# Kernel tuning notes

Measured on AMD Instinct MI355X. Metric: run time of the kernel, lower is better.

## Reference

```python
import jax, jax.numpy as jnp
import numpy as np
import math

B, N, D = 8, 4096, 256
Q = 0.5
K = 8  # max_order
EPS = 1e-5


def scale_norm(x, g):
    n = jnp.linalg.norm(x, axis=-1, keepdims=True)
    return g * x / jnp.maximum(n, EPS)


def siren(x, w1, b1, g, w2, b2):
    # nn.Linear uses y = x @ W.T + b with W [out, in]
    h = jnp.sin(jnp.einsum('bnd,ed->bne', x, w1) + b1)
    h = scale_norm(h, g)
    return jnp.sin(jnp.einsum('bnd,ed->bne', h, w2) + b2)


def adaptive_avg_pool6(x):
    # AdaptiveAvgPool1d(6) over last dim (torch semantics: bin j = mean(x[floor(jL/6):ceil((j+1)L/6)]))
    L = x.shape[-1]
    cols = []
    for j in range(6):
        s = (j * L) // 6
        e = -((-(j + 1) * L) // 6)
        cols.append(jnp.mean(x[..., s:e], axis=-1))
    return jnp.stack(cols, axis=-1)


def jackson_damp(k_max):
    c = math.pi / (k_max + 2)
    k = np.arange(k_max + 1)
    d = ((k_max + 2 - k) * math.sin(c) * np.cos(k * c) + math.cos(c) * np.sin(k * c)) / ((k_max + 2) * math.sin(c))
    d[0] = 1.0
    return jnp.asarray(d, dtype=jnp.float32)


def cheb_gibbs(seq, coef, damp):
    # seq [B,N], coef [B,K+1], damp [K+1] (rows of module buffer are identical)
    out = coef[:, 0:1] + seq * coef[:, 1:2] * damp[1]
    tx0, tx1 = jnp.ones_like(seq), seq
    for k in range(2, K + 1):
        tx2 = 2.0 * seq * tx1 - tx0
        out = out + tx2 * coef[:, k:k + 1] * damp[k]
        tx0, tx1 = tx1, tx2
    return out


def givens(alpha, beta, gamma):
    ra = (alpha + beta) * (math.pi / 2.0)
    rs = (alpha - beta) * (math.pi / 2.0)
    gm = gamma * (math.pi / 2.0)
    cg, sg = jnp.cos(gm), jnp.sin(gm)
    g_ii = jnp.exp(-1j * ra) * cg
    g_ij = jnp.exp(-1j * rs) * sg
    g_ji = -jnp.exp(1j * rs) * sg
    g_jj = jnp.exp(1j * ra) * cg
    return g_ii, g_ij, g_ji, g_jj


def dhhp(x, li, lij, lji, ljj, ui, uij, uji, ujj, diag_pre=None, diag_post=None):
    # x [B,N,D] complex; Givens factors [B,N-1]. Banded Hessenberg transform Z = G_l (G_u x).
    if diag_pre is not None:
        x = diag_pre[:, :, None] * x
    y0 = ui[:, 0:1, None] * x[:, 0:1] + uij[:, 0:1, None] * x[:, 1:2]
    ym = (uji[:, :-1, None] * x[:, :-2]
          + (ujj[:, :-1] * ui[:, 1:])[:, :, None] * x[:, 1:-1]
          + (ujj[:, :-1] * uij[:, 1:])[:, :, None] * x[:, 2:])
    yl = uji[:, -1:, None] * x[:, -2:-1] + ujj[:, -1:, None] * x[:, -1:]
    Y = jnp.concatenate([y0, ym, yl], axis=1)
    z0 = li[:, 0:1, None] * Y[:, 0:1] + lij[:, 0:1, None] * Y[:, 1:2]
    zm = ((li[:, 1:] * lji[:, :-1])[:, :, None] * Y[:, :-2]
          + (li[:, 1:] * ljj[:, :-1])[:, :, None] * Y[:, 1:-1]
          + lij[:, 1:, None] * Y[:, 2:])
    zl = lji[:, -1:, None] * Y[:, -2:-1] + ljj[:, -1:, None] * Y[:, -1:]
    Z = jnp.concatenate([z0, zm, zl], axis=1)
    if diag_post is not None:
        Z = diag_post[:, :, None] * Z
    return Z


def chsyconv(x, ev_w1, ev_b1, ev_g, ev_w2, ev_b2, hp_w1, hp_b1, hp_g, hp_w2, hp_b2, cheb_coef):
    # eigenvalue hypernetwork: mean over feat dim (pool_dim=2) -> [B,N]
    eig = jnp.mean(siren(x, ev_w1, ev_b1, ev_g, ev_w2, ev_b2), axis=2)
    filt = cheb_gibbs(eig, cheb_coef, jackson_damp(K))  # KPM-filtered eigenvalues
    diag = filt.astype(jnp.complex64) * jnp.exp(2j * math.pi * Q * eig)  # magnetic complex diagonal
    # eigenvector hyperparameters: pool feat->6, view [B,6N], chunk into 6 along dim 1
    pooled = adaptive_avg_pool6(siren(x, hp_w1, hp_b1, hp_g, hp_w2, hp_b2)).reshape(B, 6 * N)
    a_l, b_l, g_l, a_u, b_u, g_u = jnp.split(pooled, 6, axis=1)
    l_ii, l_ij, l_ji, l_jj = givens(a_l[:, 1:], b_l[:, 1:], g_l[:, 1:])
    u_ii, u_ij, u_ji, u_jj = givens(a_u[:, :-1], b_u[:, :-1], g_u[:, :-1])
    xc = x.astype(jnp.complex64)
    # DHHP transform (transform=True): diagonal filter applied after the banded transform
    Z = dhhp(xc, l_ii, l_ij, l_ji, l_jj, u_ii, u_ij, u_ji, u_jj, diag_post=diag)
    # inverse DHHP: conjugate-transpose Givens factors (ii<->jj, ij->-ij, ji->-ji), no diagonal
    out = dhhp(Z, l_jj, -l_ij, -l_ji, l_ii, u_jj, -u_ij, -u_ji, u_ii)
    return out  # complex64 [B,N,D] (value dropout is identity in eval)


def setup_inputs():
    key = jax.random.key(0)
    ks = jax.random.split(key, 5)
    bound = math.sqrt(6.0 / D)
    x = jax.random.normal(ks[0], (B, N, D), dtype=jnp.float32)
    ev_w1 = jax.random.uniform(ks[1], (D, D), jnp.float32, -bound, bound)
    ev_w2 = jax.random.uniform(ks[2], (D, D), jnp.float32, -bound, bound)
    hp_w1 = jax.random.uniform(ks[3], (D, D), jnp.float32, -bound, bound)
    hp_w2 = jax.random.uniform(ks[4], (D, D), jnp.float32, -bound, bound)
    zb = jnp.zeros((D,), jnp.float32)
    g = jnp.asarray(math.sqrt(D), jnp.float32)  # ScaleNorm scale init
    cheb_coef = jnp.full((B, K + 1), 2.0 / (K + 1), jnp.float32).at[:, 0].set(1.0 / (K + 1))
    return {"x": x, "ev_w1": ev_w1, "ev_b1": zb, "ev_g": g, "ev_w2": ev_w2, "ev_b2": zb,
            "hp_w1": hp_w1, "hp_b1": zb, "hp_g": g, "hp_w2": hp_w2, "hp_b2": zb,
            "cheb_coef": cheb_coef}


def reference(x, ev_w1, ev_b1, ev_g, ev_w2, ev_b2, hp_w1, hp_b1, hp_g, hp_w2, hp_b2, cheb_coef):
    return chsyconv(x, ev_w1, ev_b1, ev_g, ev_w2, ev_b2, hp_w1, hp_b1, hp_g, hp_w2, hp_b2, cheb_coef)
```

## Files before the change

### kernel.cpp

```cpp
#include <hip/hip_runtime.h>
#include <math.h>

typedef __attribute__((ext_vector_type(8))) _Float16 f16x8;
typedef __attribute__((ext_vector_type(4))) float    f32x4;

static constexpr int cB  = 8;
static constexpr int cN  = 4096;
static constexpr int cD  = 256;
static constexpr int cBN = cB * cN;
#define PI_F 3.14159265358979323846f

__device__ __forceinline__ float2 cmul(float2 a, float2 b) {
    return make_float2(a.x*b.x - a.y*b.y, a.x*b.y + a.y*b.x);
}
__device__ __forceinline__ float2 cfma2(float2 a, float2 b, float2 acc) {
    acc.x += a.x*b.x - a.y*b.y;
    acc.y += a.x*b.y + a.y*b.x;
    return acc;
}
__device__ __forceinline__ float2 cneg(float2 a) { return make_float2(-a.x, -a.y); }

struct G4 { float2 ii, ij, ji, jj; };

__device__ __forceinline__ G4 givens_f(float al, float be, float ga) {
    float ra = (al + be) * (PI_F * 0.5f);
    float rs = (al - be) * (PI_F * 0.5f);
    float gm = ga * (PI_F * 0.5f);
    float sg, cg, sra, cra, srs, crs;
    sincosf(gm, &sg, &cg);
    sincosf(ra, &sra, &cra);
    sincosf(rs, &srs, &crs);
    G4 g;
    g.ii = make_float2( cra*cg, -sra*cg);
    g.ij = make_float2( crs*sg, -srs*sg);
    g.ji = make_float2(-crs*sg, -srs*sg);
    g.jj = make_float2( cra*cg,  sra*cg);
    return g;
}

__global__ void sentinel_kernel(float* out, int n, float v) {
    if (n > 0) out[0] = v;
    if (n > 1) out[1] = v;
}

__global__ __launch_bounds__(256) void wcvt_kernel(
    const float* __restrict__ w0, const float* __restrict__ w1,
    const float* __restrict__ w2, const float* __restrict__ w3,
    _Float16* __restrict__ W16)
{
    int i = blockIdx.x * 256 + threadIdx.x;
    const float* src[4] = {w0, w1, w2, w3};
    #pragma unroll
    for (int m = 0; m < 4; ++m)
        W16[(size_t)m*65536 + i] = (_Float16)src[m][i];
}

__device__ __forceinline__ void stage_x16(const float* __restrict__ xrow0,
                                          _Float16* buf, int tid)
{
    const int row = tid >> 3;
    const int c0  = (tid & 7) * 32;
    const float4* src = (const float4*)(xrow0 + row*256 + c0);
    const int swz = (row & 7) << 4;
    #pragma unroll
    for (int j = 0; j < 4; ++j) {
        float4 p = src[2*j], q = src[2*j+1];
        f16x8 h;
        h[0]=(_Float16)p.x; h[1]=(_Float16)p.y; h[2]=(_Float16)p.z; h[3]=(_Float16)p.w;
        h[4]=(_Float16)q.x; h[5]=(_Float16)q.y; h[6]=(_Float16)q.z; h[7]=(_Float16)q.w;
        int off = (((c0 + j*8) * 2) ^ swz);
        *(f16x8*)((char*)buf + row*512 + off) = h;
    }
}

__device__ __forceinline__ void ld_a1(const _Float16* src, int k0, int lr, int kq,
                                      f16x8 ah[4])
{
    #pragma unroll
    for (int mt = 0; mt < 4; ++mt) {
        int row = mt*16 + lr;
        int off = ((k0*2 + kq*16) ^ ((row & 7) << 4));
        ah[mt] = *(const f16x8*)((const char*)src + row*512 + off);
    }
}

__device__ __forceinline__ void ld_w1(const _Float16* __restrict__ wP,
                                      int k0, int w, int lr, int kq, f16x8 bh[2])
{
    #pragma unroll
    for (int nt = 0; nt < 2; ++nt) {
        int col = w*32 + nt*16 + lr;
        bh[nt] = *(const f16x8*)(wP + col*256 + k0 + kq*8);
    }
}

__device__ __forceinline__ void do_mfma8(const f16x8 ah[4], const f16x8 bh[2],
                                         f32x4 acc[4][2])
{
    #pragma unroll
    for (int mt = 0; mt < 4; ++mt)
        #pragma unroll
        for (int nt = 0; nt < 2; ++nt)
            acc[mt][nt] = __builtin_amdgcn_mfma_f32_16x16x32_f16(ah[mt], bh[nt], acc[mt][nt], 0, 0, 0);
}

__device__ __forceinline__ void gemm32(const _Float16* aSrc,
                                       const _Float16* __restrict__ wP,
                                       int w, int lr, int kq, f32x4 acc[4][2])
{
    f16x8 ah[4];
    f16x8 b0[2], b1[2];
    ld_w1(wP, 0, w, lr, kq, b0);
    #pragma unroll
    for (int kk = 0; kk < 8; ++kk) {
        ld_a1(aSrc, kk*32, lr, kq, ah);
        if ((kk & 1) == 0) {
            if (kk < 7) ld_w1(wP, (kk+1)*32, w, lr, kq, b1);
            do_mfma8(ah, b0, acc);
        } else {
            if (kk < 7) ld_w1(wP, (kk+1)*32, w, lr, kq, b0);
            do_mfma8(ah, b1, acc);
        }
    }
}

__global__ __launch_bounds__(512, 2) void siren_mfma(
    const float* __restrict__ x, const _Float16* __restrict__ W16,
    const float* __restrict__ ev_b1, const float* __restrict__ ev_g,
    const float* __restrict__ ev_b2,
    const float* __restrict__ hp_b1, const float* __restrict__ hp_g,
    const float* __restrict__ hp_b2,
    const float* __restrict__ cheb,
    float* __restrict__ Pout, float2* __restrict__ DIAG)
{
    __shared__ _Float16 buf[64*256];
    __shared__ float red[8][64];

    const int tid  = threadIdx.x;
    const int w    = tid >> 6;
    const int lane = tid & 63;
    const int lr   = lane & 15;
    const int kq   = lane >> 4;
    const size_t r0 = (size_t)blockIdx.x * 64;
    const int b   = (int)(r0 >> 12);
    const int net = blockIdx.y;

    const _Float16* w1P = W16 + (size_t)(net*2 + 0)*65536;
    const _Float16* w2P = W16 + (size_t)(net*2 + 1)*65536;
    const float* b1 = net ? hp_b1 : ev_b1;
    const float* b2 = net ? hp_b2 : ev_b2;
    const float  g  = net ? hp_g[0] : ev_g[0];

    stage_x16(x + r0*256, buf, tid);
    __syncthreads();

    f32x4 acc[4][2];
    #pragma unroll
    for (int mt = 0; mt < 4; ++mt)
        #pragma unroll
        for (int nt = 0; nt < 2; ++nt) acc[mt][nt] = (f32x4)(0.f);
    gemm32(buf, w1P, w, lr, kq, acc);

    {
        float bv[2] = { b1[w*32 + lr], b1[w*32 + 16 + lr] };
        float sv[4][2][4], rn[4][4];
        #pragma unroll
        for (int mt = 0; mt < 4; ++mt)
            #pragma unroll
            for (int r = 0; r < 4; ++r) {
                float s = 0.f;
                #pragma unroll
                for (int nt = 0; nt < 2; ++nt) {
                    float v = __sinf(acc[mt][nt][r] + bv[nt]);
                    sv[mt][nt][r] = v;
                    s += v*v;
                }
                rn[mt][r] = s;
            }
        #pragma unroll
        for (int mk = 1; mk < 16; mk <<= 1)
            #pragma unroll
            for (int mt = 0; mt < 4; ++mt)
                #pragma unroll
                for (int r = 0; r < 4; ++r) rn[mt][r] += __shfl_xor(rn[mt][r], mk);
        if (lr == 0)
            #pragma unroll
            for (int mt = 0; mt < 4; ++mt)
                #pragma unroll
                for (int r = 0; r < 4; ++r) red[w][mt*16 + kq*4 + r] = rn[mt][r];
        __syncthreads();
        #pragma unroll
        for (int mt = 0; mt < 4; ++mt)
            #pragma unroll
            for (int r = 0; r < 4; ++r) {
                int row = mt*16 + kq*4 + r;
                float tot = 0.f;
                #pragma unroll
                for (int ww = 0; ww < 8; ++ww) tot += red[ww][row];
                float sc = g / fmaxf(sqrtf(tot), 1e-5f);
                int swz = (row & 7) << 4;
                #pragma unroll
                for (int nt = 0; nt < 2; ++nt) {
                    float v = sv[mt][nt][r] * sc;
                    int col = w*32 + nt*16 + lr;
                    *(_Float16*)((char*)buf + row*512 + ((col*2) ^ swz)) = (_Float16)v;
                }
            }
    }
    __syncthreads();

    #pragma unroll
    for (int mt = 0; mt < 4; ++mt)
        #pragma unroll
        for (int nt = 0; nt < 2; ++nt) acc[mt][nt] = (f32x4)(0.f);
    gemm32(buf, w2P, w, lr, kq, acc);

    if (net == 0) {
        float bv[2] = { b2[w*32 + lr], b2[w*32 + 16 + lr] };
        float es[4][4];
        #pragma unroll
        for (int mt = 0; mt < 4; ++mt)
            #pragma unroll
            for (int r = 0; r < 4; ++r) {
                float s = 0.f;
                #pragma unroll
                for (int nt = 0; nt < 2; ++nt) s += __sinf(acc[mt][nt][r] + bv[nt]);
                es[mt][r] = s;
            }
        #pragma unroll
        for (int mk = 1; mk < 16; mk <<= 1)
            #pragma unroll
            for (int mt = 0; mt < 4; ++mt)
                #pragma unroll
                for (int r = 0; r < 4; ++r) es[mt][r] += __shfl_xor(es[mt][r], mk);
        if (lr == 0)
            #pragma unroll
            for (int mt = 0; mt < 4; ++mt)
                #pragma unroll
                for (int r = 0; r < 4; ++r) red[w][mt*16 + kq*4 + r] = es[mt][r];
        __syncthreads();
        if (tid < 64) {
            int row = tid;
            float tot = 0.f;
            #pragma unroll
            for (int ww = 0; ww < 8; ++ww) tot += red[ww][row];
            float ev = tot * (1.f/256.f);
            float dmp[9];
            {
                const double c = 3.14159265358979323846 / 10.0;
                double sc = sin(c), cc = cos(c);
                dmp[0] = 1.f;
                for (int k = 1; k < 9; ++k)
                    dmp[k] = (float)(((10.0 - k) * sc * cos(k*c) + cc * sin(k*c)) / (10.0 * sc));
            }
            const float* cf = cheb + b*9;
            float t0 = 1.f, t1 = ev;
            float filt = cf[0] + ev * cf[1] * dmp[1];
            #pragma unroll
            for (int k = 2; k < 9; ++k) {
                float t2 = 2.f*ev*t1 - t0;
                filt += t2 * cf[k] * dmp[k];
                t0 = t1; t1 = t2;
            }
            float sp, cp;
            sincosf(PI_F * ev, &sp, &cp);
            DIAG[r0 + row] = make_float2(filt*cp, filt*sp);
        }
    } else {
        __syncthreads();
        float bv[2] = { b2[w*32 + lr], b2[w*32 + 16 + lr] };
        #pragma unroll
        for (int mt = 0; mt < 4; ++mt)
            #pragma unroll
            for (int r = 0; r < 4; ++r) {
                int row = mt*16 + kq*4 + r;
                int swz = (row & 7) << 4;
                #pragma unroll
                for (int nt = 0; nt < 2; ++nt) {
                    float v = __sinf(acc[mt][nt][r] + bv[nt]);
                    int col = w*32 + nt*16 + lr;
                    *(_Float16*)((char*)buf + row*512 + ((col*2) ^ swz)) = (_Float16)v;
                }
            }
        __syncthreads();
        if (tid < 384) {
            const int sb[6] = {0, 42, 85, 128, 170, 213};
            const int eb[6] = {43, 86, 128, 171, 214, 256};
            const float inv[6] = {1.f/43.f, 1.f/44.f, 1.f/43.f, 1.f/43.f, 1.f/44.f, 1.f/43.f};
            int row = tid / 6, q = tid - row*6;
            int swz = (row & 7) << 4;
            float s = 0.f;
            for (int c = sb[q]; c < eb[q]; ++c)
                s += (float)(*(const _Float16*)((const char*)buf + row*512 + ((c*2) ^ swz)));
            int nn = (int)(r0 & 4095) + row;
            Pout[(size_t)b*6*cN + nn*6 + q] = s * inv[q];
        }
    }
}

__global__ __launch_bounds__(256) void prep_T(
    const float* __restrict__ P, const float2* __restrict__ DIAG,
    float2* __restrict__ T)
{
    __shared__ G4 uL[266], lL[266];
    __shared__ float2 dgL[262];

    const int tid = threadIdx.x;
    const int m0 = (blockIdx.x & 15) * 256;
    const int b  = blockIdx.x >> 4;
    const size_t bbase = (size_t)b * cN;
    const int b6 = b * 6 * cN;
    const float2 z2 = make_float2(0.f, 0.f);
    const int jb = m0 - 5;

    for (int t = tid; t < 265; t += 256) {
        int j = jb + t;
        G4 gu, gl;
        gu.ii = gu.ij = gu.ji = gu.jj = z2; gl = gu;
        if (j >= 0 && j <= cN-2) {
            gu = givens_f(P[b6+3*cN+j], P[b6+4*cN+j], P[b6+5*cN+j]);
            gl = givens_f(P[b6+j+1],    P[b6+cN+j+1], P[b6+2*cN+j+1]);
        }
        uL[t] = gu; lL[t] = gl;
    }
    for (int t = tid; t < 261; t += 256) {
        int m = m0 - 2 + t;
        dgL[t] = (m >= 0 && m < cN) ? DIAG[bbase + m] : z2;
    }
    __syncthreads();

    const int m = m0 + tid;
    auto scoef = [&](int s, int rr, float2& A, float2& B, float2& C) {
        A = z2; B = z2; C = z2;
        if (rr < 0 || rr >= cN) return;
        if (s == 1) {
            if (rr == 0)         { G4 u0 = uL[0-jb]; B = u0.ii; C = u0.ij; }
            else if (rr == cN-1) { G4 up = uL[rr-1-jb]; A = up.ji; B = up.jj; }
            else { G4 up = uL[rr-1-jb], uc = uL[rr-jb];
                   A = up.ji; B = cmul(up.jj, uc.ii); C = cmul(up.jj, uc.ij); }
        } else if (s == 2) {
            if (rr == 0)         { G4 l0 = lL[0-jb]; B = l0.ii; C = l0.ij; }
            else if (rr == cN-1) { G4 lp = lL[rr-1-jb]; A = lp.ji; B = lp.jj; }
            else { G4 lp = lL[rr-1-jb], lc = lL[rr-jb];
                   A = cmul(lc.ii, lp.ji); B = cmul(lc.ii, lp.jj); C = lc.ij; }
        } else if (s == 3) {
            if (rr == 0)         { G4 u0 = uL[0-jb]; B = u0.jj; C = cneg(u0.ij); }
            else if (rr == cN-1) { G4 up = uL[rr-1-jb]; A = cneg(up.ji); B = up.ii; }
            else { G4 up = uL[rr-1-jb], uc = uL[rr-jb];
                   A = cneg(up.ji); B = cmul(up.ii, uc.jj); C = cneg(cmul(up.ii, uc.ij)); }
        } else {
            if (rr == 0)         { G4 l0 = lL[0-jb]; B = l0.jj; C = cneg(l0.ij); }
            else if (rr == cN-1) { G4 lp = lL[rr-1-jb]; A = cneg(lp.ji); B = lp.ii; }
            else { G4 lp = lL[rr-1-jb], lc = lL[rr-jb];
                   A = cneg(cmul(lc.jj, lp.ji)); B = cmul(lc.jj, lp.ii); C = cneg(lc.ij); }
        }
    };

    float2 wv[9], nw[9];
    #pragma unroll
    for (int k = 0; k < 9; ++k) wv[k] = z2;
    {
        float2 A, B, C; scoef(4, m, A, B, C);
        wv[3] = A; wv[4] = B; wv[5] = C;
    }
    #pragma unroll
    for (int k = 0; k < 9; ++k) nw[k] = z2;
    #pragma unroll
    for (int i = 3; i <= 5; ++i) {
        float2 A, B, C; scoef(3, m + i - 4, A, B, C);
        nw[i-1] = cfma2(wv[i], A, nw[i-1]);
        nw[i]   = cfma2(wv[i], B, nw[i]);
        nw[i+1] = cfma2(wv[i], C, nw[i+1]);
    }
    #pragma unroll
    for (int k = 0; k < 9; ++k) wv[k] = nw[k];
    #pragma unroll
    for (int k = 2; k <= 6; ++k) wv[k] = cmul(wv[k], dgL[tid + k - 2]);
    #pragma unroll
    for (int k = 0; k < 9; ++k) nw[k] = z2;
    #pragma unroll
    for (int i = 2; i <= 6; ++i) {
        float2 A, B, C; scoef(2, m + i - 4, A, B, C);
        nw[i-1] = cfma2(wv[i], A, nw[i-1]);
        nw[i]   = cfma2(wv[i], B, nw[i]);
        nw[i+1] = cfma2(wv[i], C, nw[i+1]);
    }
    #pragma unroll
    for (int k = 0; k < 9; ++k) wv[k] = nw[k];
    #pragma unroll
    for (int k = 0; k < 9; ++k) nw[k] = z2;
    #pragma unroll
    for (int i = 1; i <= 7; ++i) {
        float2 A, B, C; scoef(1, m + i - 4, A, B, C);
        nw[i-1] = cfma2(wv[i], A, nw[i-1]);
        nw[i]   = cfma2(wv[i], B, nw[i]);
        nw[i+1] = cfma2(wv[i], C, nw[i+1]);
    }
    #pragma unroll
    for (int k = 0; k < 9; ++k) T[(bbase + m)*9 + k] = nw[k];
}

__global__ __launch_bounds__(256) void dhhp_stencil(
    const float* __restrict__ x, const float2* __restrict__ T,
    float* __restrict__ outf, unsigned long long out_floats, int mode)
{
    __shared__ float  xsr[40*256];
    __shared__ float2 cT[32][9];

    const int tid = threadIdx.x;
    const int n0 = blockIdx.x * 32;
    const int b  = blockIdx.y;
    const size_t bbase = (size_t)b * cN;

    for (int idx = tid; idx < 40*64; idx += 256) {
        int r = idx >> 6, d4 = idx & 63;
        int m = n0 - 4 + r;
        float4 v = make_float4(0.f, 0.f, 0.f, 0.f);
        if (m >= 0 && m < cN) v = *(const float4*)(x + (bbase + m)*cD + d4*4);
        *(float4*)(xsr + r*256 + d4*4) = v;
    }
    for (int idx = tid; idx < 288; idx += 256) {
        int r = idx / 9, j = idx - r*9;
        cT[r][j] = T[(bbase + n0 + r)*9 + j];
    }
    __syncthreads();

    for (int idx = tid; idx < 32*64; idx += 256) {
        int r = idx >> 6, d4 = idx & 63;
        float4 ox = make_float4(0.f, 0.f, 0.f, 0.f);
        float4 oy = make_float4(0.f, 0.f, 0.f, 0.f);
        #pragma unroll
        for (int j = 0; j < 9; ++j) {
            float4 xv = *(const float4*)(xsr + (r + j)*256 + d4*4);
            float2 t = cT[r][j];
            ox.x = fmaf(t.x, xv.x, ox.x); ox.y = fmaf(t.x, xv.y, ox.y);
            ox.z = fmaf(t.x, xv.z, ox.z); ox.w = fmaf(t.x, xv.w, ox.w);
            oy.x = fmaf(t.y, xv.x, oy.x); oy.y = fmaf(t.y, xv.y, oy.y);
            oy.z = fmaf(t.y, xv.z, oy.z); oy.w = fmaf(t.y, xv.w, oy.w);
        }
        unsigned long long ci = (unsigned long long)((bbase + n0 + r)*(size_t)cD + d4*4);
        if (mode == 0) {
            if (ci + 4ULL <= out_floats) *(float4*)(outf + ci) = ox;
        } else {
            if (2ULL*(ci + 4ULL) <= out_floats) {
                float2* o2 = (float2*)outf + ci;
                o2[0] = make_float2(ox.x, oy.x);
                o2[1] = make_float2(ox.y, oy.y);
                o2[2] = make_float2(ox.z, oy.z);
                o2[3] = make_float2(ox.w, oy.w);
            }
        }
    }
}

extern "C" void kernel_launch(void* const* d_in, const int* in_sizes, int n_in,
                              void* d_out, int out_size, void* d_ws, size_t ws_size,
                              hipStream_t stream)
{
    const int expect[12] = { cBN*cD, cD*cD, cD, 1, cD*cD, cD,
                             cD*cD, cD, 1, cD*cD, cD, cB*9 };
    bool ok = (n_in == 12);
    if (ok) for (int i = 0; i < 12; ++i) ok = ok && (in_sizes[i] == expect[i]);
    if (!ok) {
        sentinel_kernel<<<1, 1, 0, stream>>>((float*)d_out, out_size, 1.0e6f);
        return;
    }
    const size_t pBytes = (size_t)cB * 6 * cN * sizeof(float);
    const size_t dBytes = (size_t)cBN * sizeof(float2);
    const size_t wBytes = (size_t)4 * 65536 * sizeof(_Float16);
    const size_t tBytes = (size_t)cBN * 9 * sizeof(float2);
    if (d_ws == nullptr || ws_size < pBytes + dBytes + wBytes + tBytes) {
        sentinel_kernel<<<1, 1, 0, stream>>>((float*)d_out, out_size, 2.0e6f);
        return;
    }
    int mode;
    if (out_size == cBN * cD)          mode = 0;
    else if (out_size == 2 * cBN * cD) mode = 1;
    else {
        sentinel_kernel<<<1, 1, 0, stream>>>((float*)d_out, out_size, 3.0e6f);
        return;
    }

    const float* x     = (const float*)d_in[0];
    const float* ev_w1 = (const float*)d_in[1];
    const float* ev_b1 = (const float*)d_in[2];
    const float* ev_g  = (const float*)d_in[3];
    const float* ev_w2 = (const float*)d_in[4];
    const float* ev_b2 = (const float*)d_in[5];
    const float* hp_w1 = (const float*)d_in[6];
    const float* hp_b1 = (const float*)d_in[7];
    const float* hp_g  = (const float*)d_in[8];
    const float* hp_w2 = (const float*)d_in[9];
    const float* hp_b2 = (const float*)d_in[10];
    const float* cheb  = (const float*)d_in[11];

    float*     P    = (float*)d_ws;
    float2*    DIAG = (float2*)((char*)d_ws + pBytes);
    _Float16*  W16  = (_Float16*)((char*)d_ws + pBytes + dBytes);
    float2*    T    = (float2*)((char*)d_ws + pBytes + dBytes + wBytes);

    wcvt_kernel<<<dim3(256), 256, 0, stream>>>(ev_w1, ev_w2, hp_w1, hp_w2, W16);
    siren_mfma<<<dim3(cBN/64, 2), 512, 0, stream>>>(x, W16, ev_b1, ev_g, ev_b2,
                                                    hp_b1, hp_g, hp_b2, cheb, P, DIAG);
    prep_T<<<dim3(cB * (cN/256)), 256, 0, stream>>>(P, DIAG, T);
    dhhp_stencil<<<dim3(cN/32, cB), 256, 0, stream>>>(x, T, (float*)d_out,
                                                      (unsigned long long)out_size,
                                                      mode);
}
```

Measured before the change: 84.45 us.

## Fuse stencil coefficient prep into dhhp_stencil and recompute sine instead of storing

```diff
diff --git a/kernel.cpp b/kernel.cpp
--- a/kernel.cpp
+++ b/kernel.cpp
@@ -163,7 +163,7 @@
 
     {
         float bv[2] = { b1[w*32 + lr], b1[w*32 + 16 + lr] };
-        float sv[4][2][4], rn[4][4];
+        float rn[4][4];
         #pragma unroll
         for (int mt = 0; mt < 4; ++mt)
             #pragma unroll
@@ -172,7 +172,6 @@
                 #pragma unroll
                 for (int nt = 0; nt < 2; ++nt) {
                     float v = __sinf(acc[mt][nt][r] + bv[nt]);
-                    sv[mt][nt][r] = v;
                     s += v*v;
                 }
                 rn[mt][r] = s;
@@ -201,7 +200,7 @@
                 int swz = (row & 7) << 4;
                 #pragma unroll
                 for (int nt = 0; nt < 2; ++nt) {
-                    float v = sv[mt][nt][r] * sc;
+                    float v = __sinf(acc[mt][nt][r] + bv[nt]) * sc;
                     int col = w*32 + nt*16 + lr;
                     *(_Float16*)((char*)buf + row*512 + ((col*2) ^ swz)) = (_Float16)v;
                 }
@@ -298,119 +297,23 @@
     }
 }
 
-__global__ __launch_bounds__(256) void prep_T(
-    const float* __restrict__ P, const float2* __restrict__ DIAG,
-    float2* __restrict__ T)
-{
-    __shared__ G4 uL[266], lL[266];
-    __shared__ float2 dgL[262];
-
-    const int tid = threadIdx.x;
-    const int m0 = (blockIdx.x & 15) * 256;
-    const int b  = blockIdx.x >> 4;
-    const size_t bbase = (size_t)b * cN;
-    const int b6 = b * 6 * cN;
-    const float2 z2 = make_float2(0.f, 0.f);
-    const int jb = m0 - 5;
-
-    for (int t = tid; t < 265; t += 256) {
-        int j = jb + t;
-        G4 gu, gl;
-        gu.ii = gu.ij = gu.ji = gu.jj = z2; gl = gu;
-        if (j >= 0 && j <= cN-2) {
-            gu = givens_f(P[b6+3*cN+j], P[b6+4*cN+j], P[b6+5*cN+j]);
-            gl = givens_f(P[b6+j+1],    P[b6+cN+j+1], P[b6+2*cN+j+1]);
-        }
-        uL[t] = gu; lL[t] = gl;
-    }
-    for (int t = tid; t < 261; t += 256) {
-        int m = m0 - 2 + t;
-        dgL[t] = (m >= 0 && m < cN) ? DIAG[bbase + m] : z2;
-    }
-    __syncthreads();
-
-    const int m = m0 + tid;
-    auto scoef = [&](int s, int rr, float2& A, float2& B, float2& C) {
-        A = z2; B = z2; C = z2;
-        if (rr < 0 || rr >= cN) return;
-        if (s == 1) {
-            if (rr == 0)         { G4 u0 = uL[0-jb]; B = u0.ii; C = u0.ij; }
-            else if (rr == cN-1) { G4 up = uL[rr-1-jb]; A = up.ji; B = up.jj; }
-            else { G4 up = uL[rr-1-jb], uc = uL[rr-jb];
-                   A = up.ji; B = cmul(up.jj, uc.ii); C = cmul(up.jj, uc.ij); }
-        } else if (s == 2) {
-            if (rr == 0)         { G4 l0 = lL[0-jb]; B = l0.ii; C = l0.ij; }
-            else if (rr == cN-1) { G4 lp = lL[rr-1-jb]; A = lp.ji; B = lp.jj; }
-            else { G4 lp = lL[rr-1-jb], lc = lL[rr-jb];
-                   A = cmul(lc.ii, lp.ji); B = cmul(lc.ii, lp.jj); C = lc.ij; }
-        } else if (s == 3) {
-            if (rr == 0)         { G4 u0 = uL[0-jb]; B = u0.jj; C = cneg(u0.ij); }
-            else if (rr == cN-1) { G4 up = uL[rr-1-jb]; A = cneg(up.ji); B = up.ii; }
-            else { G4 up = uL[rr-1-jb], uc = uL[rr-jb];
-                   A = cneg(up.ji); B = cmul(up.ii, uc.jj); C = cneg(cmul(up.ii, uc.ij)); }
-        } else {
-            if (rr == 0)         { G4 l0 = lL[0-jb]; B = l0.jj; C = cneg(l0.ij); }
-            else if (rr == cN-1) { G4 lp = lL[rr-1-jb]; A = cneg(lp.ji); B = lp.ii; }
-            else { G4 lp = lL[rr-1-jb], lc = lL[rr-jb];
-                   A = cneg(cmul(lc.jj, lp.ji)); B = cmul(lc.jj, lp.ii); C = cneg(lc.ij); }
-        }
-    };
-
-    float2 wv[9], nw[9];
-    #pragma unroll
-    for (int k = 0; k < 9; ++k) wv[k] = z2;
-    {
-        float2 A, B, C; scoef(4, m, A, B, C);
-        wv[3] = A; wv[4] = B; wv[5] = C;
-    }
-    #pragma unroll
-    for (int k = 0; k < 9; ++k) nw[k] = z2;
-    #pragma unroll
-    for (int i = 3; i <= 5; ++i) {
-        float2 A, B, C; scoef(3, m + i - 4, A, B, C);
-        nw[i-1] = cfma2(wv[i], A, nw[i-1]);
-        nw[i]   = cfma2(wv[i], B, nw[i]);
-        nw[i+1] = cfma2(wv[i], C, nw[i+1]);
-    }
-    #pragma unroll
-    for (int k = 0; k < 9; ++k) wv[k] = nw[k];
-    #pragma unroll
-    for (int k = 2; k <= 6; ++k) wv[k] = cmul(wv[k], dgL[tid + k - 2]);
-    #pragma unroll
-    for (int k = 0; k < 9; ++k) nw[k] = z2;
-    #pragma unroll
-    for (int i = 2; i <= 6; ++i) {
-        float2 A, B, C; scoef(2, m + i - 4, A, B, C);
-        nw[i-1] = cfma2(wv[i], A, nw[i-1]);
-        nw[i]   = cfma2(wv[i], B, nw[i]);
-        nw[i+1] = cfma2(wv[i], C, nw[i+1]);
-    }
-    #pragma unroll
-    for (int k = 0; k < 9; ++k) wv[k] = nw[k];
-    #pragma unroll
-    for (int k = 0; k < 9; ++k) nw[k] = z2;
-    #pragma unroll
-    for (int i = 1; i <= 7; ++i) {
-        float2 A, B, C; scoef(1, m + i - 4, A, B, C);
-        nw[i-1] = cfma2(wv[i], A, nw[i-1]);
-        nw[i]   = cfma2(wv[i], B, nw[i]);
-        nw[i+1] = cfma2(wv[i], C, nw[i+1]);
-    }
-    #pragma unroll
-    for (int k = 0; k < 9; ++k) T[(bbase + m)*9 + k] = nw[k];
-}
-
 __global__ __launch_bounds__(256) void dhhp_stencil(
-    const float* __restrict__ x, const float2* __restrict__ T,
-    float* __restrict__ outf, unsigned long long out_floats, int mode)
+    const float* __restrict__ x, const float* __restrict__ P,
+    const float2* __restrict__ DIAG, float* __restrict__ outf,
+    unsigned long long out_floats, int mode)
 {
     __shared__ float  xsr[40*256];
+    __shared__ G4 uG[41], lG[41];
+    __shared__ float2 cDg[40];
     __shared__ float2 cT[32][9];
 
     const int tid = threadIdx.x;
     const int n0 = blockIdx.x * 32;
     const int b  = blockIdx.y;
     const size_t bbase = (size_t)b * cN;
+    const int b6 = b * 6 * cN;
+    const float2 z2 = make_float2(0.f, 0.f);
+    const int jb = n0 - 5;
 
     for (int idx = tid; idx < 40*64; idx += 256) {
         int r = idx >> 6, d4 = idx & 63;
@@ -419,9 +322,92 @@
         if (m >= 0 && m < cN) v = *(const float4*)(x + (bbase + m)*cD + d4*4);
         *(float4*)(xsr + r*256 + d4*4) = v;
     }
-    for (int idx = tid; idx < 288; idx += 256) {
-        int r = idx / 9, j = idx - r*9;
-        cT[r][j] = T[(bbase + n0 + r)*9 + j];
+    if (tid < 82) {
+        int t = (tid < 41) ? tid : tid - 41;
+        int j = jb + t;
+        G4 g; g.ii = g.ij = g.ji = g.jj = z2;
+        if (j >= 0 && j <= cN-2) {
+            if (tid < 41) g = givens_f(P[b6+3*cN+j], P[b6+4*cN+j], P[b6+5*cN+j]);
+            else          g = givens_f(P[b6+j+1],    P[b6+cN+j+1], P[b6+2*cN+j+1]);
+        }
+        if (tid < 41) uG[t] = g; else lG[t] = g;
+    } else if (tid < 122) {
+        int t = tid - 82;
+        int m = n0 - 4 + t;
+        cDg[t] = (m >= 0 && m < cN) ? DIAG[bbase + m] : z2;
+    }
+    __syncthreads();
+
+    if (tid < 32) {
+        const int m = n0 + tid;
+        auto scoef = [&](int s, int rr, float2& A, float2& B, float2& C) {
+            A = z2; B = z2; C = z2;
+            if (rr < 0 || rr >= cN) return;
+            if (s == 1) {
+                if (rr == 0)         { G4 u0 = uG[0-jb]; B = u0.ii; C = u0.ij; }
+                else if (rr == cN-1) { G4 up = uG[rr-1-jb]; A = up.ji; B = up.jj; }
+                else { G4 up = uG[rr-1-jb], uc = uG[rr-jb];
+                       A = up.ji; B = cmul(up.jj, uc.ii); C = cmul(up.jj, uc.ij); }
+            } else if (s == 2) {
+                if (rr == 0)         { G4 l0 = lG[0-jb]; B = l0.ii; C = l0.ij; }
+                else if (rr == cN-1) { G4 lp = lG[rr-1-jb]; A = lp.ji; B = lp.jj; }
+                else { G4 lp = lG[rr-1-jb], lc = lG[rr-jb];
+                       A = cmul(lc.ii, lp.ji); B = cmul(lc.ii, lp.jj); C = lc.ij; }
+            } else if (s == 3) {
+                if (rr == 0)         { G4 u0 = uG[0-jb]; B = u0.jj; C = cneg(u0.ij); }
+                else if (rr == cN-1) { G4 up = uG[rr-1-jb]; A = cneg(up.ji); B = up.ii; }
+                else { G4 up = uG[rr-1-jb], uc = uG[rr-jb];
+                       A = cneg(up.ji); B = cmul(up.ii, uc.jj); C = cneg(cmul(up.ii, uc.ij)); }
+            } else {
+                if (rr == 0)         { G4 l0 = lG[0-jb]; B = l0.jj; C = cneg(l0.ij); }
+                else if (rr == cN-1) { G4 lp = lG[rr-1-jb]; A = cneg(lp.ji); B = lp.ii; }
+                else { G4 lp = lG[rr-1-jb], lc = lG[rr-jb];
+                       A = cneg(cmul(lc.jj, lp.ji)); B = cmul(lc.jj, lp.ii); C = cneg(lc.ij); }
+            }
+        };
+
+        float2 wv[9], nw[9];
+        #pragma unroll
+        for (int k = 0; k < 9; ++k) wv[k] = z2;
+        {
+            float2 A, B, C; scoef(4, m, A, B, C);
+            wv[3] = A; wv[4] = B; wv[5] = C;
+        }
+        #pragma unroll
+        for (int k = 0; k < 9; ++k) nw[k] = z2;
+        #pragma unroll
+        for (int i = 3; i <= 5; ++i) {
+            float2 A, B, C; scoef(3, m + i - 4, A, B, C);
+            nw[i-1] = cfma2(wv[i], A, nw[i-1]);
+            nw[i]   = cfma2(wv[i], B, nw[i]);
+            nw[i+1] = cfma2(wv[i], C, nw[i+1]);
+        }
+        #pragma unroll
+        for (int k = 0; k < 9; ++k) wv[k] = nw[k];
+        #pragma unroll
+        for (int k = 2; k <= 6; ++k) wv[k] = cmul(wv[k], cDg[tid + k]);
+        #pragma unroll
+        for (int k = 0; k < 9; ++k) nw[k] = z2;
+        #pragma unroll
+        for (int i = 2; i <= 6; ++i) {
+            float2 A, B, C; scoef(2, m + i - 4, A, B, C);
+            nw[i-1] = cfma2(wv[i], A, nw[i-1]);
+            nw[i]   = cfma2(wv[i], B, nw[i]);
+            nw[i+1] = cfma2(wv[i], C, nw[i+1]);
+        }
+        #pragma unroll
+        for (int k = 0; k < 9; ++k) wv[k] = nw[k];
+        #pragma unroll
+        for (int k = 0; k < 9; ++k) nw[k] = z2;
+        #pragma unroll
+        for (int i = 1; i <= 7; ++i) {
+            float2 A, B, C; scoef(1, m + i - 4, A, B, C);
+            nw[i-1] = cfma2(wv[i], A, nw[i-1]);
+            nw[i]   = cfma2(wv[i], B, nw[i]);
+            nw[i+1] = cfma2(wv[i], C, nw[i+1]);
+        }
+        #pragma unroll
+        for (int k = 0; k < 9; ++k) cT[tid][k] = nw[k];
     }
     __syncthreads();
 
@@ -468,8 +454,7 @@
     const size_t pBytes = (size_t)cB * 6 * cN * sizeof(float);
     const size_t dBytes = (size_t)cBN * sizeof(float2);
     const size_t wBytes = (size_t)4 * 65536 * sizeof(_Float16);
-    const size_t tBytes = (size_t)cBN * 9 * sizeof(float2);
-    if (d_ws == nullptr || ws_size < pBytes + dBytes + wBytes + tBytes) {
+    if (d_ws == nullptr || ws_size < pBytes + dBytes + wBytes) {
         sentinel_kernel<<<1, 1, 0, stream>>>((float*)d_out, out_size, 2.0e6f);
         return;
     }
@@ -497,13 +482,11 @@
     float*     P    = (float*)d_ws;
     float2*    DIAG = (float2*)((char*)d_ws + pBytes);
     _Float16*  W16  = (_Float16*)((char*)d_ws + pBytes + dBytes);
-    float2*    T    = (float2*)((char*)d_ws + pBytes + dBytes + wBytes);
 
     wcvt_kernel<<<dim3(256), 256, 0, stream>>>(ev_w1, ev_w2, hp_w1, hp_w2, W16);
     siren_mfma<<<dim3(cBN/64, 2), 512, 0, stream>>>(x, W16, ev_b1, ev_g, ev_b2,
                                                     hp_b1, hp_g, hp_b2, cheb, P, DIAG);
-    prep_T<<<dim3(cB * (cN/256)), 256, 0, stream>>>(P, DIAG, T);
-    dhhp_stencil<<<dim3(cN/32, cB), 256, 0, stream>>>(x, T, (float*)d_out,
+    dhhp_stencil<<<dim3(cN/32, cB), 256, 0, stream>>>(x, P, DIAG, (float*)d_out,
                                                       (unsigned long long)out_size,
                                                       mode);
 }
```

Result: no change. 83.61 us (median of 2 runs) (-1.0%).
